# Optimization experiments

Measured on AMD Instinct MI355X. Metric: run time of the kernel, lower is better.

## Reference

```python
import jax, jax.numpy as jnp
import numpy as np

N = 50000      # nodes
E = 800000     # edges
P = 100000     # pos/neg candidate edges
IN = 128       # input feat dim
H, D = 2, 64   # heads, out_feats per head
HD = H * D     # 128
NEG_SLOPE = 0.2


def setup_inputs() -> dict:
    key = jax.random.key(0)
    ks = jax.random.split(key, 18)
    def gn(k, shape, fan_in):
        return jax.random.normal(k, shape, jnp.float32) * (1.0 / np.sqrt(fan_in))
    return {
        "x": jax.random.normal(ks[0], (N, IN), jnp.float32),
        "src": jax.random.randint(ks[1], (E,), 0, N),
        "dst": jax.random.randint(ks[2], (E,), 0, N),
        "pos_src": jax.random.randint(ks[3], (P,), 0, N),
        "pos_dst": jax.random.randint(ks[4], (P,), 0, N),
        "neg_src": jax.random.randint(ks[5], (P,), 0, N),
        "neg_dst": jax.random.randint(ks[6], (P,), 0, N),
        "W0": gn(ks[7], (IN, HD), IN),
        "attn0": gn(ks[8], (H, D), D),
        "W1": gn(ks[9], (HD, HD), HD),
        "attn1": gn(ks[10], (H, D), D),
        "Wp1": gn(ks[11], (HD, D), HD),
        "bp1": jnp.zeros((D,), jnp.float32),
        "Wp2": gn(ks[12], (D, D), D),
        "bp2": jnp.zeros((D,), jnp.float32),
        "Wp3": gn(ks[13], (D, 1), D),
        "bp3": jnp.zeros((1,), jnp.float32),
    }


def gatv2_layer(h, W, attn, src, dst, residual):
    # DGL GATv2Conv, share_weights=True, bias=False, feat_drop=attn_drop=0
    feat = (h @ W).reshape(N, H, D)            # [N,H,D]
    el = feat[src]                              # [E,H,D] gather at src
    er = feat[dst]                              # [E,H,D] gather at dst
    e = jax.nn.leaky_relu(el + er, NEG_SLOPE)   # [E,H,D]
    score = jnp.einsum('ehd,hd->eh', e, attn)   # [E,H]
    # edge softmax over incoming edges of each dst node
    m = jax.ops.segment_max(score, dst, num_segments=N)      # [N,H]
    p = jnp.exp(score - m[dst])                               # [E,H]
    s = jax.ops.segment_sum(p, dst, num_segments=N)           # [N,H]
    a = p / s[dst]                                             # [E,H]
    rst = jax.ops.segment_sum(el * a[:, :, None], dst, num_segments=N)  # [N,H,D]
    if residual:
        rst = rst + h.reshape(N, H, D)          # identity res_fc (dims match)
    return jax.nn.elu(rst).reshape(N, HD)       # flatten(1)


def reference(x, src, dst, pos_src, pos_dst, neg_src, neg_dst,
              W0, attn0, W1, attn1, Wp1, bp1, Wp2, bp2, Wp3, bp3):
    h = gatv2_layer(x, W0, attn0, src, dst, residual=False)
    h = gatv2_layer(h, W1, attn1, src, dst, residual=True)

    def predictor(z):
        z = jax.nn.relu(z @ Wp1 + bp1)
        z = jax.nn.relu(z @ Wp2 + bp2)
        return z @ Wp3 + bp3

    h_pos = predictor(h[pos_src] * h[pos_dst])  # [P,1]
    h_neg = predictor(h[neg_src] * h[neg_dst])  # [P,1]
    return (h_pos, h_neg)
```

## Files before the change

### kernel.cpp

```cpp
#include <hip/hip_runtime.h>
#include <math.h>

#define NN 50000
#define NE 800000
#define NP 100000
#define NEG_SLOPE 0.2f
#define SCAN_NB 196

__device__ __forceinline__ float row_sum16(float v) {
    int x = __float_as_int(v);
    v += __int_as_float(__builtin_amdgcn_update_dpp(0, x, 0x128, 0xF, 0xF, true));
    x = __float_as_int(v);
    v += __int_as_float(__builtin_amdgcn_update_dpp(0, x, 0x124, 0xF, 0xF, true));
    x = __float_as_int(v);
    v += __int_as_float(__builtin_amdgcn_update_dpp(0, x, 0x4E, 0xF, 0xF, true));
    x = __float_as_int(v);
    v += __int_as_float(__builtin_amdgcn_update_dpp(0, x, 0xB1, 0xF, 0xF, true));
    return v;
}


__global__ void count_deg(const int* __restrict__ dst, int* __restrict__ cnt) {
    int i = blockIdx.x * blockDim.x + threadIdx.x;
    int st = gridDim.x * blockDim.x;
    const int4* d4 = (const int4*)dst;
    for (; i < NE / 4; i += st) {
        int4 d = d4[i];
        atomicAdd(&cnt[d.x], 1);
        atomicAdd(&cnt[d.y], 1);
        atomicAdd(&cnt[d.z], 1);
        atomicAdd(&cnt[d.w], 1);
    }
}

__global__ __launch_bounds__(256) void scan_part(const int* __restrict__ cnt,
                                                 int* __restrict__ partial) {
    __shared__ int ws[4];
    int t = threadIdx.x;
    int idx = blockIdx.x * 256 + t;
    int v = (idx < NN) ? cnt[idx] : 0;
    #pragma unroll
    for (int mm = 1; mm < 64; mm <<= 1) v += __shfl_xor(v, mm, 64);
    if ((t & 63) == 0) ws[t >> 6] = v;
    __syncthreads();
    if (t == 0) partial[blockIdx.x] = ws[0] + ws[1] + ws[2] + ws[3];
}

__global__ __launch_bounds__(256) void scan_top(const int* __restrict__ partial,
                                                int* __restrict__ partoff,
                                                int* __restrict__ rowptr) {
    __shared__ int wsum[4];
    int t = threadIdx.x, lane = t & 63, w = t >> 6;
    int v = (t < SCAN_NB) ? partial[t] : 0;
    int x = v;
    #pragma unroll
    for (int mm = 1; mm < 64; mm <<= 1) {
        int y = __shfl_up(x, mm, 64);
        if (lane >= mm) x += y;
    }
    if (lane == 63) wsum[w] = x;
    __syncthreads();
    int off = 0;
    for (int k = 0; k < w; ++k) off += wsum[k];
    int excl = off + x - v;
    if (t < SCAN_NB) partoff[t] = excl;
    if (t == SCAN_NB - 1) rowptr[NN] = excl + v;
}

__global__ __launch_bounds__(256) void scan_apply(const int* __restrict__ cnt,
                                                  const int* __restrict__ partoff,
                                                  int* __restrict__ rowptr,
                                                  int* __restrict__ cursor) {
    __shared__ int wsum[4];
    int t = threadIdx.x, lane = t & 63, w = t >> 6;
    int idx = blockIdx.x * 256 + t;
    int v = (idx < NN) ? cnt[idx] : 0;
    int x = v;
    #pragma unroll
    for (int mm = 1; mm < 64; mm <<= 1) {
        int y = __shfl_up(x, mm, 64);
        if (lane >= mm) x += y;
    }
    if (lane == 63) wsum[w] = x;
    __syncthreads();
    int off = partoff[blockIdx.x];
    for (int k = 0; k < w; ++k) off += wsum[k];
    int excl = off + x - v;
    if (idx < NN) { rowptr[idx] = excl; cursor[idx] = excl; }
}

__global__ void scatter_edges(const int* __restrict__ src, const int* __restrict__ dst,
                              int* __restrict__ cursor, int* __restrict__ csrc) {
    int i = blockIdx.x * blockDim.x + threadIdx.x;
    int st = gridDim.x * blockDim.x;
    const int4* s4 = (const int4*)src;
    const int4* d4 = (const int4*)dst;
    for (; i < NE / 4; i += st) {
        int4 s = s4[i];
        int4 d = d4[i];
        int p;
        p = atomicAdd(&cursor[d.x], 1); csrc[p] = s.x;
        p = atomicAdd(&cursor[d.y], 1); csrc[p] = s.y;
        p = atomicAdd(&cursor[d.z], 1); csrc[p] = s.z;
        p = atomicAdd(&cursor[d.w], 1); csrc[p] = s.w;
    }
}


__global__ __launch_bounds__(256) void gemm128(const float* __restrict__ A,
                                               const float* __restrict__ W,
                                               float* __restrict__ out, int nrows) {
    __shared__ float Wt[128 * 132];
    __shared__ float rb[16 * 132];
    int tid = threadIdx.x;
    for (int idx = tid; idx < 128 * 128; idx += 256) {
        int k = idx >> 7, j = idx & 127;
        Wt[j * 132 + k] = W[idx];
    }
    __syncthreads();
    int lane = tid & 63, w = tid >> 6;
    int ntiles = (nrows + 15) >> 4;
    const float* w0p = &Wt[lane * 132];
    const float* w1p = &Wt[(64 + lane) * 132];
    for (int t = blockIdx.x; t < ntiles; t += gridDim.x) {
        int r0 = t << 4;
        for (int i = tid; i < 512; i += 256) {
            int rr = r0 + (i >> 5);
            float4 v = {0.f, 0.f, 0.f, 0.f};
            if (rr < nrows) v = ((const float4*)A)[(size_t)rr * 32 + (i & 31)];
            *(float4*)&rb[(i >> 5) * 132 + (i & 31) * 4] = v;
        }
        __syncthreads();
        float acc[4][2] = {};
        #pragma unroll 4
        for (int k4 = 0; k4 < 32; ++k4) {
            float4 wv0 = *(const float4*)&w0p[k4 * 4];
            float4 wv1 = *(const float4*)&w1p[k4 * 4];
            #pragma unroll
            for (int i2 = 0; i2 < 4; ++i2) {
                float4 av = *(const float4*)&rb[(w * 4 + i2) * 132 + k4 * 4];
                acc[i2][0] = fmaf(av.x, wv0.x, acc[i2][0]);
                acc[i2][0] = fmaf(av.y, wv0.y, acc[i2][0]);
                acc[i2][0] = fmaf(av.z, wv0.z, acc[i2][0]);
                acc[i2][0] = fmaf(av.w, wv0.w, acc[i2][0]);
                acc[i2][1] = fmaf(av.x, wv1.x, acc[i2][1]);
                acc[i2][1] = fmaf(av.y, wv1.y, acc[i2][1]);
                acc[i2][1] = fmaf(av.z, wv1.z, acc[i2][1]);
                acc[i2][1] = fmaf(av.w, wv1.w, acc[i2][1]);
            }
        }
        #pragma unroll
        for (int i2 = 0; i2 < 4; ++i2) {
            int rr = r0 + w * 4 + i2;
            if (rr < nrows) {
                out[(size_t)rr * 128 + lane]      = acc[i2][0];
                out[(size_t)rr * 128 + 64 + lane] = acc[i2][1];
            }
        }
        __syncthreads();
    }
}


#define GAT_EDGE(fv) do {                                          \
    float ex = fv.x + fd.x; ex = fmaxf(ex, NEG_SLOPE * ex);        \
    float ey = fv.y + fd.y; ey = fmaxf(ey, NEG_SLOPE * ey);        \
    float ez = fv.z + fd.z; ez = fmaxf(ez, NEG_SLOPE * ez);        \
    float ew = fv.w + fd.w; ew = fmaxf(ew, NEG_SLOPE * ew);        \
    float part = ex * at.x + ey * at.y + ez * at.z + ew * at.w;    \
    part = row_sum16(part);                                        \
    float p = __expf(part - m);                                    \
    s += p;                                                        \
    ax = fmaf(fv.x, p, ax);                                        \
    ay = fmaf(fv.y, p, ay);                                        \
    az = fmaf(fv.z, p, az);                                        \
    aw = fmaf(fv.w, p, aw);                                        \
} while (0)

__global__ void gat_fused(const float* __restrict__ feat,
                          const int* __restrict__ rowptr,
                          const int* __restrict__ csrc,
                          const float* __restrict__ attn,
                          const float* __restrict__ resid,
                          float* __restrict__ out) {
    int tid = blockIdx.x * blockDim.x + threadIdx.x;
    int hw = tid >> 5;
    int nhw = (gridDim.x * blockDim.x) >> 5;
    int q = threadIdx.x & 31;
    const float4* feat4 = (const float4*)feat;
    float4 at = ((const float4*)attn)[q];
    for (int d = hw; d < NN; d += nhw) {
        int beg = rowptr[d], end = rowptr[d + 1];
        float4 fd = feat4[(size_t)d * 32 + q];
        float m = 0.f, s = 0.f;
        float ax = 0.f, ay = 0.f, az = 0.f, aw = 0.f;
        int i = beg;
        float4 f0 = {0.f,0.f,0.f,0.f}, f1 = {0.f,0.f,0.f,0.f}, f2 = {0.f,0.f,0.f,0.f};
        int s3 = 0;
        if (i < end) {
            int p0 = csrc[i];
            int p1 = (i + 1 < end) ? csrc[i + 1] : 0;
            int p2 = (i + 2 < end) ? csrc[i + 2] : 0;
            int p3 = (i + 3 < end) ? csrc[i + 3] : 0;
            s3     = (i + 4 < end) ? csrc[i + 4] : 0;
            float4 fp = feat4[(size_t)p0 * 32 + q];
            if (i + 1 < end) f0 = feat4[(size_t)p1 * 32 + q];
            if (i + 2 < end) f1 = feat4[(size_t)p2 * 32 + q];
            if (i + 3 < end) f2 = feat4[(size_t)p3 * 32 + q];
            float ex = fp.x + fd.x; ex = fmaxf(ex, NEG_SLOPE * ex);
            float ey = fp.y + fd.y; ey = fmaxf(ey, NEG_SLOPE * ey);
            float ez = fp.z + fd.z; ez = fmaxf(ez, NEG_SLOPE * ez);
            float ew = fp.w + fd.w; ew = fmaxf(ew, NEG_SLOPE * ew);
            float part = ex * at.x + ey * at.y + ez * at.z + ew * at.w;
            m = row_sum16(part);
            s = 1.f;
            ax = fp.x; ay = fp.y; az = fp.z; aw = fp.w;
            ++i;
        }
        while (i + 8 <= end) {
            int s4 = csrc[i + 4];
            int s5 = csrc[i + 5];
            int s6 = csrc[i + 6];
            int s7 = csrc[i + 7];
            float4 f3 = feat4[(size_t)s3 * 32 + q];
            GAT_EDGE(f0);
            f0 = feat4[(size_t)s4 * 32 + q];
            GAT_EDGE(f1);
            f1 = feat4[(size_t)s5 * 32 + q];
            GAT_EDGE(f2);
            f2 = feat4[(size_t)s6 * 32 + q];
            GAT_EDGE(f3);
            s3 = s7;
            i += 4;
        }
        while (i < end) {
            float4 f3 = {0.f, 0.f, 0.f, 0.f};
            if (i + 3 < end) f3 = feat4[(size_t)s3 * 32 + q];
            int s4 = (i + 4 < end) ? csrc[i + 4] : 0;
            GAT_EDGE(f0);
            f0 = f1; f1 = f2; f2 = f3; s3 = s4; ++i;
        }
        float inv = s > 0.f ? 1.f / s : 0.f;
        float vx = ax * inv;
        float vy = ay * inv;
        float vz = az * inv;
        float vw = aw * inv;
        if (resid) {
            float4 r = ((const float4*)resid)[(size_t)d * 32 + q];
            vx += r.x; vy += r.y; vz += r.z; vw += r.w;
        }
        vx = vx > 0.f ? vx : expm1f(vx);
        vy = vy > 0.f ? vy : expm1f(vy);
        vz = vz > 0.f ? vz : expm1f(vz);
        vw = vw > 0.f ? vw : expm1f(vw);
        float4 o; o.x = vx; o.y = vy; o.z = vz; o.w = vw;
        ((float4*)out)[(size_t)d * 32 + q] = o;
    }
}


__global__ __launch_bounds__(512, 1) void predictor(const float* __restrict__ h,
                          const int* __restrict__ ps, const int* __restrict__ pd,
                          const int* __restrict__ ns, const int* __restrict__ nd,
                          const float* __restrict__ Wp1, const float* __restrict__ bp1,
                          const float* __restrict__ Wp2, const float* __restrict__ bp2,
                          const float* __restrict__ Wp3, const float* __restrict__ bp3,
                          float* __restrict__ out) {
    __shared__ float S[29696];
    int tid = threadIdx.x;
    for (int idx = tid; idx < 128 * 64; idx += 512) {
        int k = idx >> 6, c = idx & 63;
        S[c * 132 + k] = Wp1[idx];
    }
    for (int idx = tid; idx < 64 * 64; idx += 512) {
        int k = idx >> 6, c = idx & 63;
        S[8448 + c * 68 + k] = Wp2[idx];
    }
    __syncthreads();
    int lane = tid & 63;
    int w = tid >> 6;
    int cg = lane & 15, rg = lane >> 4;
    float* zz = S + 12800 + w * 2112;
    float b1v[4], b2v[4], w3v[4];
    #pragma unroll
    for (int i = 0; i < 4; ++i) {
        b1v[i] = bp1[cg + 16 * i];
        b2v[i] = bp2[cg + 16 * i];
        w3v[i] = Wp3[cg + 16 * i];
    }
    float b3 = bp3[0];
    int gw = blockIdx.x * 8 + w;
    int gnw = gridDim.x * 8;
    int ge = lane >> 2, gp = lane & 3;
    const float4* h4 = (const float4*)h;
    const int NT = (2 * NP) / 16;
    for (int T = gw; T < NT; T += gnw) {
        int e = T * 16 + ge;
        int a, b;
        if (e < NP) { a = ps[e]; b = pd[e]; }
        else        { a = ns[e - NP]; b = nd[e - NP]; }
        const float4* pa = h4 + (size_t)a * 32 + gp;
        const float4* pb = h4 + (size_t)b * 32 + gp;
        #pragma unroll
        for (int qq = 0; qq < 8; ++qq) {
            float4 va = pa[qq * 4];
            float4 vb = pb[qq * 4];
            float4 vz;
            vz.x = va.x * vb.x; vz.y = va.y * vb.y;
            vz.z = va.z * vb.z; vz.w = va.w * vb.w;
            *(float4*)&zz[ge * 132 + gp * 4 + qq * 16] = vz;
        }
        float acc[4][4] = {};
        #pragma unroll 4
        for (int k4 = 0; k4 < 32; ++k4) {
            float4 wv[4], zv[4];
            #pragma unroll
            for (int i = 0; i < 4; ++i)
                wv[i] = *(const float4*)&S[(cg + 16 * i) * 132 + k4 * 4];
            #pragma unroll
            for (int j = 0; j < 4; ++j)
                zv[j] = *(const float4*)&zz[(rg * 4 + j) * 132 + k4 * 4];
            #pragma unroll
            for (int j = 0; j < 4; ++j) {
                #pragma unroll
                for (int i = 0; i < 4; ++i) {
                    acc[j][i] = fmaf(zv[j].x, wv[i].x, acc[j][i]);
                    acc[j][i] = fmaf(zv[j].y, wv[i].y, acc[j][i]);
                    acc[j][i] = fmaf(zv[j].z, wv[i].z, acc[j][i]);
                    acc[j][i] = fmaf(zv[j].w, wv[i].w, acc[j][i]);
                }
            }
        }
        #pragma unroll
        for (int j = 0; j < 4; ++j) {
            #pragma unroll
            for (int i = 0; i < 4; ++i)
                zz[(rg * 4 + j) * 68 + cg + 16 * i] = fmaxf(acc[j][i] + b1v[i], 0.f);
        }
        float acc2[4][4] = {};
        #pragma unroll 4
        for (int k4 = 0; k4 < 16; ++k4) {
            float4 wv[4], zv[4];
            #pragma unroll
            for (int i = 0; i < 4; ++i)
                wv[i] = *(const float4*)&S[8448 + (cg + 16 * i) * 68 + k4 * 4];
            #pragma unroll
            for (int j = 0; j < 4; ++j)
                zv[j] = *(const float4*)&zz[(rg * 4 + j) * 68 + k4 * 4];
            #pragma unroll
            for (int j = 0; j < 4; ++j) {
                #pragma unroll
                for (int i = 0; i < 4; ++i) {
                    acc2[j][i] = fmaf(zv[j].x, wv[i].x, acc2[j][i]);
                    acc2[j][i] = fmaf(zv[j].y, wv[i].y, acc2[j][i]);
                    acc2[j][i] = fmaf(zv[j].z, wv[i].z, acc2[j][i]);
                    acc2[j][i] = fmaf(zv[j].w, wv[i].w, acc2[j][i]);
                }
            }
        }
        float v[4];
        #pragma unroll
        for (int j = 0; j < 4; ++j) {
            float sv = 0.f;
            #pragma unroll
            for (int i = 0; i < 4; ++i)
                sv = fmaf(fmaxf(acc2[j][i] + b2v[i], 0.f), w3v[i], sv);
            v[j] = row_sum16(sv);
        }
        if (cg == 0) {
            float4 o;
            o.x = v[0] + b3; o.y = v[1] + b3; o.z = v[2] + b3; o.w = v[3] + b3;
            *(float4*)&out[T * 16 + rg * 4] = o;
        }
    }
}

extern "C" void kernel_launch(void* const* d_in, const int* in_sizes, int n_in,
                              void* d_out, int out_size, void* d_ws, size_t ws_size,
                              hipStream_t stream) {
    const float* x       = (const float*)d_in[0];
    const int*   src     = (const int*)d_in[1];
    const int*   dst     = (const int*)d_in[2];
    const int*   pos_src = (const int*)d_in[3];
    const int*   pos_dst = (const int*)d_in[4];
    const int*   neg_src = (const int*)d_in[5];
    const int*   neg_dst = (const int*)d_in[6];
    const float* W0      = (const float*)d_in[7];
    const float* attn0   = (const float*)d_in[8];
    const float* W1      = (const float*)d_in[9];
    const float* attn1   = (const float*)d_in[10];
    const float* Wp1     = (const float*)d_in[11];
    const float* bp1     = (const float*)d_in[12];
    const float* Wp2     = (const float*)d_in[13];
    const float* bp2     = (const float*)d_in[14];
    const float* Wp3     = (const float*)d_in[15];
    const float* bp3     = (const float*)d_in[16];

    float* A = (float*)d_ws;
    float* B = A + (size_t)NN * 128;
    float* C = B + (size_t)NN * 128;
    int* cnt     = (int*)(C + (size_t)NN * 128);
    int* rowptr  = cnt + NN;
    int* cursor  = rowptr + NN + 1;
    int* csrc    = cursor + NN;
    int* partial = csrc + NE;
    int* partoff = partial + SCAN_NB;
    float* out = (float*)d_out;

    hipMemsetAsync(cnt, 0, NN * sizeof(int), stream);
    count_deg<<<782, 256, 0, stream>>>(dst, cnt);
    scan_part<<<SCAN_NB, 256, 0, stream>>>(cnt, partial);
    scan_top<<<1, 256, 0, stream>>>(partial, partoff, rowptr);
    scan_apply<<<SCAN_NB, 256, 0, stream>>>(cnt, partoff, rowptr, cursor);
    scatter_edges<<<782, 256, 0, stream>>>(src, dst, cursor, csrc);

    gemm128<<<1024, 256, 0, stream>>>(x, W0, A, NN);
    gat_fused<<<3125, 256, 0, stream>>>(A, rowptr, csrc, attn0, nullptr, C);

    gemm128<<<1024, 256, 0, stream>>>(C, W1, A, NN);
    gat_fused<<<3125, 256, 0, stream>>>(A, rowptr, csrc, attn1, C, B);

    predictor<<<256, 512, 0, stream>>>(B, pos_src, pos_dst, neg_src, neg_dst,
                                       Wp1, bp1, Wp2, bp2, Wp3, bp3, out);
}
```

Baseline: 388.9 us.

## Read GEMM A rows via uniform scalar loads and split predictor launch

The gemm128 kernel no longer stages 16 rows of A in shared memory behind a barrier. Each wave instead reads its 4 rows directly from global memory through a wave-uniform base address, so the compiler can use scalar loads, and the per-tile barriers go away. The tail bounds check is dropped, which relies on nrows being a multiple of 16 (50000 is). The predictor launch is split into two launches over halves of the tile range, adding one launch of overhead with no clear benefit.

```diff
diff --git a/kernel.cpp b/kernel.cpp
--- a/kernel.cpp
+++ b/kernel.cpp
@@ -111,7 +111,6 @@
                                                const float* __restrict__ W,
                                                float* __restrict__ out, int nrows) {
     __shared__ float Wt[128 * 132];
-    __shared__ float rb[16 * 132];
     int tid = threadIdx.x;
     for (int idx = tid; idx < 128 * 128; idx += 256) {
         int k = idx >> 7, j = idx & 127;
@@ -119,45 +118,43 @@
     }
     __syncthreads();
     int lane = tid & 63, w = tid >> 6;
-    int ntiles = (nrows + 15) >> 4;
+    int ntiles = nrows >> 4;
     const float* w0p = &Wt[lane * 132];
     const float* w1p = &Wt[(64 + lane) * 132];
     for (int t = blockIdx.x; t < ntiles; t += gridDim.x) {
-        int r0 = t << 4;
-        for (int i = tid; i < 512; i += 256) {
-            int rr = r0 + (i >> 5);
-            float4 v = {0.f, 0.f, 0.f, 0.f};
-            if (rr < nrows) v = ((const float4*)A)[(size_t)rr * 32 + (i & 31)];
-            *(float4*)&rb[(i >> 5) * 132 + (i & 31) * 4] = v;
-        }
-        __syncthreads();
+        int rbu = __builtin_amdgcn_readfirstlane((t << 4) + w * 4);
+        const float* a0 = A + (size_t)rbu * 128;
+        const float* a1 = a0 + 128;
+        const float* a2 = a0 + 256;
+        const float* a3 = a0 + 384;
         float acc[4][2] = {};
         #pragma unroll 4
         for (int k4 = 0; k4 < 32; ++k4) {
             float4 wv0 = *(const float4*)&w0p[k4 * 4];
             float4 wv1 = *(const float4*)&w1p[k4 * 4];
-            #pragma unroll
-            for (int i2 = 0; i2 < 4; ++i2) {
-                float4 av = *(const float4*)&rb[(w * 4 + i2) * 132 + k4 * 4];
-                acc[i2][0] = fmaf(av.x, wv0.x, acc[i2][0]);
-                acc[i2][0] = fmaf(av.y, wv0.y, acc[i2][0]);
-                acc[i2][0] = fmaf(av.z, wv0.z, acc[i2][0]);
-                acc[i2][0] = fmaf(av.w, wv0.w, acc[i2][0]);
-                acc[i2][1] = fmaf(av.x, wv1.x, acc[i2][1]);
-                acc[i2][1] = fmaf(av.y, wv1.y, acc[i2][1]);
-                acc[i2][1] = fmaf(av.z, wv1.z, acc[i2][1]);
-                acc[i2][1] = fmaf(av.w, wv1.w, acc[i2][1]);
+            int kb = k4 * 4;
+            const float* ap[4] = {a0, a1, a2, a3};
+            #pragma unroll
+            for (int j = 0; j < 4; ++j) {
+                float A0 = ap[j][kb + 0];
+                float A1 = ap[j][kb + 1];
+                float A2 = ap[j][kb + 2];
+                float A3 = ap[j][kb + 3];
+                acc[j][0] = fmaf(A0, wv0.x, acc[j][0]);
+                acc[j][0] = fmaf(A1, wv0.y, acc[j][0]);
+                acc[j][0] = fmaf(A2, wv0.z, acc[j][0]);
+                acc[j][0] = fmaf(A3, wv0.w, acc[j][0]);
+                acc[j][1] = fmaf(A0, wv1.x, acc[j][1]);
+                acc[j][1] = fmaf(A1, wv1.y, acc[j][1]);
+                acc[j][1] = fmaf(A2, wv1.z, acc[j][1]);
+                acc[j][1] = fmaf(A3, wv1.w, acc[j][1]);
             }
         }
         #pragma unroll
-        for (int i2 = 0; i2 < 4; ++i2) {
-            int rr = r0 + w * 4 + i2;
-            if (rr < nrows) {
-                out[(size_t)rr * 128 + lane]      = acc[i2][0];
-                out[(size_t)rr * 128 + 64 + lane] = acc[i2][1];
-            }
-        }
-        __syncthreads();
+        for (int j = 0; j < 4; ++j) {
+            out[(size_t)(rbu + j) * 128 + lane]      = acc[j][0];
+            out[(size_t)(rbu + j) * 128 + 64 + lane] = acc[j][1];
+        }
     }
 }
 
@@ -265,7 +262,7 @@
                           const float* __restrict__ Wp1, const float* __restrict__ bp1,
                           const float* __restrict__ Wp2, const float* __restrict__ bp2,
                           const float* __restrict__ Wp3, const float* __restrict__ bp3,
-                          float* __restrict__ out) {
+                          int t0, int nt, float* __restrict__ out) {
     __shared__ float S[29696];
     int tid = threadIdx.x;
     for (int idx = tid; idx < 128 * 64; idx += 512) {
@@ -293,8 +290,7 @@
     int gnw = gridDim.x * 8;
     int ge = lane >> 2, gp = lane & 3;
     const float4* h4 = (const float4*)h;
-    const int NT = (2 * NP) / 16;
-    for (int T = gw; T < NT; T += gnw) {
+    for (int T = t0 + gw; T < t0 + nt; T += gnw) {
         int e = T * 16 + ge;
         int a, b;
         if (e < NP) { a = ps[e]; b = pd[e]; }
@@ -421,5 +417,7 @@
     gat_fused<<<3125, 256, 0, stream>>>(A, rowptr, csrc, attn1, C, B);
 
     predictor<<<256, 512, 0, stream>>>(B, pos_src, pos_dst, neg_src, neg_dst,
-                                       Wp1, bp1, Wp2, bp2, Wp3, bp3, out);
-}
+                                       Wp1, bp1, Wp2, bp2, Wp3, bp3, 0, 6250, out);
+    predictor<<<256, 512, 0, stream>>>(B, pos_src, pos_dst, neg_src, neg_dst,
+                                       Wp1, bp1, Wp2, bp2, Wp3, bp3, 6250, 6250, out);
+}
```

New measurement: 403.0 us. 3.6% more time.
